# Optimization experiments

Measured on AMD Instinct MI355X. Metric: run time of the kernel, lower is better.

Reference implementation:

```python
import jax, jax.numpy as jnp
import numpy as np

T = 2.0          # hardcoded in the original __init__ (ignores the arg)
EPSILON = 0.1
N_ITERS = 20     # sinkhorn_loss passes n_iters=20 to sinkhorn_normalized
SCALE = 0.001


def setup_inputs() -> dict:
    key = jax.random.key(0)
    k1, k2 = jax.random.split(key)
    B, N, C = 8, 1024, 64
    y_s = jax.random.normal(k1, (B, N, C), dtype=jnp.float32)
    y_t = jax.random.normal(k2, (B, N, C), dtype=jnp.float32)
    return {"y_s": y_s, "y_t": y_t}


def _sinkhorn_loss(x, y):
    # x, y: [N, C]. cdist p=1 -> [N, N]
    Wxy = jnp.sum(jnp.abs(x[:, None, :] - y[None, :, :]), axis=-1)  # [N, N]
    K = jnp.exp(-Wxy / EPSILON)

    def body(P, _):
        P = P / jnp.sum(P, axis=1, keepdims=True)  # row normalize
        P = P / jnp.sum(P, axis=0, keepdims=True)  # col normalize
        return P, None

    P, _ = jax.lax.scan(body, K, None, length=N_ITERS)
    return jnp.sum(P * Wxy)


def reference(y_s, y_t):
    # softmax over dim=1 (the N axis), exactly as nn.Softmax(dim=1) on [B,N,C]
    p_s = jax.nn.softmax(y_s / T, axis=1)
    p_t = jax.nn.softmax(y_t / T, axis=1)
    # original Python loop computes the loss per sample but OVERWRITES
    # emd_loss each iteration; lax.map mirrors the sequential per-sample
    # work, and we return only the last sample's loss (faithful to the bug).
    losses = jax.lax.map(lambda xy: _sinkhorn_loss(xy[0], xy[1]), (p_s, p_t))
    return SCALE * losses[-1]
```

## Files before the change

### kernel.cpp

```cpp
#include <hip/hip_runtime.h>


static constexpr int N = 1024;
static constexpr int C = 64;

static constexpr int WS_XS = 0;
static constexpr int WS_YS = 65536;
static constexpr int WS_K  = 131072;
static constexpr int WS_KT = 1179648;
static constexpr int WS_U  = 2228224;
static constexpr int WS_V  = 2229248;
static constexpr int WS_P  = 2230272;

__device__ __forceinline__ float wsum(float v) {
    #pragma unroll
    for (int o = 32; o > 0; o >>= 1) v += __shfl_down(v, o, 64);
    return v;
}
__device__ __forceinline__ float wmax(float v) {
    #pragma unroll
    for (int o = 32; o > 0; o >>= 1) v = fmaxf(v, __shfl_down(v, o, 64));
    return v;
}

__global__ void __launch_bounds__(256)
softmax_k(const float* __restrict__ ysrc, const float* __restrict__ ytrc,
          float* __restrict__ ws)
{
    __shared__ float sm[4];
    const int tid = threadIdx.x, bid = blockIdx.x;
    const int wid = tid >> 6, lane = tid & 63;
    const float* src = ((bid < C) ? ysrc : ytrc) + 7 * N * C;
    float* dst = ws + ((bid < C) ? WS_XS : WS_YS);
    const int c = bid & (C - 1);

    float vals[4];
    float m = -1e30f;
    #pragma unroll
    for (int q = 0; q < 4; ++q) {
        vals[q] = src[(q * 256 + tid) * C + c] * 0.5f;
        m = fmaxf(m, vals[q]);
    }
    m = wmax(m);
    if (lane == 0) sm[wid] = m;
    __syncthreads();
    m = fmaxf(fmaxf(sm[0], sm[1]), fmaxf(sm[2], sm[3]));
    float s = 0.f;
    #pragma unroll
    for (int q = 0; q < 4; ++q) { vals[q] = expf(vals[q] - m); s += vals[q]; }
    s = wsum(s);
    __syncthreads();
    if (lane == 0) sm[wid] = s;
    __syncthreads();
    s = sm[0] + sm[1] + sm[2] + sm[3];
    const float inv = 1.0f / s;
    #pragma unroll
    for (int q = 0; q < 4; ++q) dst[(q * 256 + tid) * C + c] = vals[q] * inv;
}

__global__ void __launch_bounds__(256)
buildK_k(float* __restrict__ ws)
{
    __shared__ float smem[5184];
    float* xs  = ws + WS_XS;
    float* ysm = ws + WS_YS;
    float* K   = ws + WS_K;
    float* KT  = ws + WS_KT;
    const int tid = threadIdx.x, bid = blockIdx.x;

    if (bid < 4) ws[WS_V + bid * 256 + tid] = 1.0f;

    float* sx = smem;
    float* sy = smem + 2048;
    float* kt = smem + 4128;
    #pragma unroll 1
    for (int t = 0; t < 4; ++t) {
        const int tt = bid * 4 + t;
        const int ti = tt >> 5, tj = tt & 31;
        __syncthreads();
        for (int k = tid; k < 2048; k += 256) sx[k] = xs[ti * 2048 + k];
        for (int k = tid; k < 2048; k += 256)
            sy[(k >> 6) * 65 + (k & 63)] = ysm[tj * 2048 + k];
        __syncthreads();
        float kv[4];
        #pragma unroll
        for (int q = 0; q < 4; ++q) {
            const int idx = q * 256 + tid;
            const int il = idx >> 5, jl = idx & 31;
            float a = 0.f;
            #pragma unroll
            for (int c = 0; c < 64; ++c)
                a += fabsf(sx[il * 64 + c] - sy[jl * 65 + c]);
            kv[q] = expf(-10.0f * a);
            K[(ti * 32 + il) * N + tj * 32 + jl] = kv[q];
        }
        __syncthreads();
        #pragma unroll
        for (int q = 0; q < 4; ++q) {
            const int idx = q * 256 + tid;
            kt[(idx >> 5) * 33 + (idx & 31)] = kv[q];
        }
        __syncthreads();
        #pragma unroll
        for (int q = 0; q < 4; ++q) {
            const int idx = q * 256 + tid;
            const int jl = idx >> 5, il = idx & 31;
            KT[(tj * 32 + jl) * N + ti * 32 + il] = kt[il * 33 + jl];
        }
    }
}

__global__ void __launch_bounds__(256)
rownorm_k(float* __restrict__ ws)
{
    const int r = blockIdx.x * 4 + (threadIdx.x >> 6);
    const int lane = threadIdx.x & 63;
    const float4* Kr4 = (const float4*)(ws + WS_K + r * N);
    const float4* v4  = (const float4*)(ws + WS_V);
    float acc = 0.f;
    #pragma unroll
    for (int j = lane; j < 256; j += 64) {
        const float4 kk = Kr4[j]; const float4 vv = v4[j];
        acc += kk.x * vv.x + kk.y * vv.y + kk.z * vv.z + kk.w * vv.w;
    }
    acc = wsum(acc);
    if (lane == 0) ws[WS_U + r] = 1.0f / acc;
}

__global__ void __launch_bounds__(256)
colnorm_k(float* __restrict__ ws)
{
    const int r = blockIdx.x * 4 + (threadIdx.x >> 6);
    const int lane = threadIdx.x & 63;
    const float4* Kr4 = (const float4*)(ws + WS_KT + r * N);
    const float4* u4  = (const float4*)(ws + WS_U);
    float acc = 0.f;
    #pragma unroll
    for (int j = lane; j < 256; j += 64) {
        const float4 kk = Kr4[j]; const float4 uu = u4[j];
        acc += kk.x * uu.x + kk.y * uu.y + kk.z * uu.z + kk.w * uu.w;
    }
    acc = wsum(acc);
    if (lane == 0) ws[WS_V + r] = 1.0f / acc;
}

__global__ void __launch_bounds__(256)
loss_partial_k(float* __restrict__ ws)
{
    __shared__ float sm[4];
    const int tid = threadIdx.x, bid = blockIdx.x;
    const int wid = tid >> 6, lane = tid & 63;
    const int r = bid * 4 + wid;
    const float* K = ws + WS_K;
    const float* v = ws + WS_V;
    float acc = 0.f;
    for (int j = lane; j < N; j += 64) {
        const float k = K[r * N + j];
        acc += k * v[j] * logf(k);
    }
    acc = wsum(acc);
    if (lane == 0) sm[wid] = ws[WS_U + r] * acc;
    __syncthreads();
    if (tid == 0) ws[WS_P + bid] = sm[0] + sm[1] + sm[2] + sm[3];
}

__global__ void __launch_bounds__(256)
loss_final_k(const float* __restrict__ ws, float* __restrict__ out)
{
    __shared__ float sm[4];
    const int tid = threadIdx.x;
    const int wid = tid >> 6, lane = tid & 63;
    float acc = ws[WS_P + tid];
    acc = wsum(acc);
    if (lane == 0) sm[wid] = acc;
    __syncthreads();
    if (tid == 0)
        out[0] = -1e-4f * (sm[0] + sm[1] + sm[2] + sm[3]);
}

extern "C" void kernel_launch(void* const* d_in, const int* in_sizes, int n_in,
                              void* d_out, int out_size, void* d_ws, size_t ws_size,
                              hipStream_t stream) {
    const float* y_s = (const float*)d_in[0];
    const float* y_t = (const float*)d_in[1];
    float* out = (float*)d_out;
    float* ws  = (float*)d_ws;

    softmax_k<<<dim3(128), dim3(256), 0, stream>>>(y_s, y_t, ws);
    buildK_k<<<dim3(256), dim3(256), 0, stream>>>(ws);
    for (int it = 0; it < 20; ++it) {
        rownorm_k<<<dim3(256), dim3(256), 0, stream>>>(ws);
        colnorm_k<<<dim3(256), dim3(256), 0, stream>>>(ws);
    }
    loss_partial_k<<<dim3(256), dim3(256), 0, stream>>>(ws);
    loss_final_k<<<dim3(1), dim3(256), 0, stream>>>(ws, out);
}
```

Before: 193.5 us.

## Fuse all stages into one persistent kernel with atomic grid barriers

Replaces the 44 separate launches (softmax, K build, 40 row/col normalisations, loss) with a single persistent kernel of 128 blocks that synchronises through an atomic-counter grid barrier, plus a tiny init kernel. Each block now processes twice as many rows and K tiles. This removes launch gaps between dependent tiny kernels. In exchange it halves the parallelism of the K build, relies on all 128 blocks being co-resident, and has a spin guard that could break out early and silently corrupt results.

```diff
diff --git a/kernel.cpp b/kernel.cpp
--- a/kernel.cpp
+++ b/kernel.cpp
@@ -1,16 +1,18 @@
 #include <hip/hip_runtime.h>
 
 
-static constexpr int N = 1024;
-static constexpr int C = 64;
-
-static constexpr int WS_XS = 0;
-static constexpr int WS_YS = 65536;
-static constexpr int WS_K  = 131072;
-static constexpr int WS_KT = 1179648;
-static constexpr int WS_U  = 2228224;
-static constexpr int WS_V  = 2229248;
-static constexpr int WS_P  = 2230272;
+static constexpr int N  = 1024;
+static constexpr int C  = 64;
+static constexpr int NB = 128;
+
+static constexpr int WS_XS  = 0;
+static constexpr int WS_YS  = 65536;
+static constexpr int WS_K   = 131072;
+static constexpr int WS_KT  = 1179648;
+static constexpr int WS_U   = 2228224;
+static constexpr int WS_V   = 2229248;
+static constexpr int WS_P   = 2230272;
+static constexpr int WS_CNT = 2230400;
 
 __device__ __forceinline__ float wsum(float v) {
     #pragma unroll
@@ -24,158 +26,179 @@
 }
 
 __global__ void __launch_bounds__(256)
-softmax_k(const float* __restrict__ ysrc, const float* __restrict__ ytrc,
-          float* __restrict__ ws)
+init_k(float* __restrict__ ws)
 {
-    __shared__ float sm[4];
-    const int tid = threadIdx.x, bid = blockIdx.x;
-    const int wid = tid >> 6, lane = tid & 63;
-    const float* src = ((bid < C) ? ysrc : ytrc) + 7 * N * C;
-    float* dst = ws + ((bid < C) ? WS_XS : WS_YS);
-    const int c = bid & (C - 1);
-
-    float vals[4];
-    float m = -1e30f;
-    #pragma unroll
-    for (int q = 0; q < 4; ++q) {
-        vals[q] = src[(q * 256 + tid) * C + c] * 0.5f;
-        m = fmaxf(m, vals[q]);
-    }
-    m = wmax(m);
-    if (lane == 0) sm[wid] = m;
-    __syncthreads();
-    m = fmaxf(fmaxf(sm[0], sm[1]), fmaxf(sm[2], sm[3]));
-    float s = 0.f;
-    #pragma unroll
-    for (int q = 0; q < 4; ++q) { vals[q] = expf(vals[q] - m); s += vals[q]; }
-    s = wsum(s);
-    __syncthreads();
-    if (lane == 0) sm[wid] = s;
-    __syncthreads();
-    s = sm[0] + sm[1] + sm[2] + sm[3];
-    const float inv = 1.0f / s;
-    #pragma unroll
-    for (int q = 0; q < 4; ++q) dst[(q * 256 + tid) * C + c] = vals[q] * inv;
+    const int tid = threadIdx.x;
+    if (tid == 0) *(int*)(ws + WS_CNT) = 0;
+    for (int i = tid; i < N; i += 256) ws[WS_V + i] = 1.0f;
 }
 
 __global__ void __launch_bounds__(256)
-buildK_k(float* __restrict__ ws)
+sink_k(const float* __restrict__ ysrc, const float* __restrict__ ytrc,
+       float* __restrict__ out, float* __restrict__ ws)
 {
     __shared__ float smem[5184];
-    float* xs  = ws + WS_XS;
-    float* ysm = ws + WS_YS;
-    float* K   = ws + WS_K;
-    float* KT  = ws + WS_KT;
-    const int tid = threadIdx.x, bid = blockIdx.x;
-
-    if (bid < 4) ws[WS_V + bid * 256 + tid] = 1.0f;
-
-    float* sx = smem;
-    float* sy = smem + 2048;
-    float* kt = smem + 4128;
+    const int tid  = threadIdx.x;
+    const int bid  = blockIdx.x;
+    const int wid  = tid >> 6;
+    const int lane = tid & 63;
+    int* cnt = (int*)(ws + WS_CNT);
+    int ep = 0;
+
+    auto gbar = [&]() {
+        __syncthreads();
+        ep += NB;
+        if (tid == 0) {
+            __hip_atomic_fetch_add(cnt, 1, __ATOMIC_RELEASE,
+                                   __HIP_MEMORY_SCOPE_AGENT);
+            int guard = 0;
+            while (__hip_atomic_load(cnt, __ATOMIC_RELAXED,
+                                     __HIP_MEMORY_SCOPE_AGENT) < ep) {
+                __builtin_amdgcn_s_sleep(2);
+                if (++guard > (1 << 22)) break;
+            }
+            __threadfence();
+        }
+        __syncthreads();
+    };
+
+    {
+        const float* src = ((bid < C) ? ysrc : ytrc) + 7 * N * C;
+        float* dst = ws + ((bid < C) ? WS_XS : WS_YS);
+        const int c = bid & (C - 1);
+        float vals[4];
+        float m = -1e30f;
+        #pragma unroll
+        for (int q = 0; q < 4; ++q) {
+            vals[q] = src[(q * 256 + tid) * C + c] * 0.5f;
+            m = fmaxf(m, vals[q]);
+        }
+        m = wmax(m);
+        if (lane == 0) smem[wid] = m;
+        __syncthreads();
+        m = fmaxf(fmaxf(smem[0], smem[1]), fmaxf(smem[2], smem[3]));
+        float s = 0.f;
+        #pragma unroll
+        for (int q = 0; q < 4; ++q) { vals[q] = expf(vals[q] - m); s += vals[q]; }
+        s = wsum(s);
+        __syncthreads();
+        if (lane == 0) smem[wid] = s;
+        __syncthreads();
+        s = smem[0] + smem[1] + smem[2] + smem[3];
+        const float inv = 1.0f / s;
+        #pragma unroll
+        for (int q = 0; q < 4; ++q) dst[(q * 256 + tid) * C + c] = vals[q] * inv;
+    }
+    gbar();
+
+    {
+        float* xs  = ws + WS_XS;
+        float* ysm = ws + WS_YS;
+        float* K   = ws + WS_K;
+        float* KT  = ws + WS_KT;
+        float* sx = smem;
+        float* sy = smem + 2048;
+        float* kt = smem + 4128;
+        #pragma unroll 1
+        for (int t = 0; t < 8; ++t) {
+            const int tt = bid * 8 + t;
+            const int ti = tt >> 5, tj = tt & 31;
+            __syncthreads();
+            for (int k = tid; k < 2048; k += 256) sx[k] = xs[ti * 2048 + k];
+            for (int k = tid; k < 2048; k += 256)
+                sy[(k >> 6) * 65 + (k & 63)] = ysm[tj * 2048 + k];
+            __syncthreads();
+            float kv[4];
+            #pragma unroll
+            for (int q = 0; q < 4; ++q) {
+                const int idx = q * 256 + tid;
+                const int il = idx >> 5, jl = idx & 31;
+                float a = 0.f;
+                #pragma unroll
+                for (int c = 0; c < 64; ++c)
+                    a += fabsf(sx[il * 64 + c] - sy[jl * 65 + c]);
+                kv[q] = expf(-10.0f * a);
+                K[(ti * 32 + il) * N + tj * 32 + jl] = kv[q];
+            }
+            __syncthreads();
+            #pragma unroll
+            for (int q = 0; q < 4; ++q) {
+                const int idx = q * 256 + tid;
+                kt[(idx >> 5) * 33 + (idx & 31)] = kv[q];
+            }
+            __syncthreads();
+            #pragma unroll
+            for (int q = 0; q < 4; ++q) {
+                const int idx = q * 256 + tid;
+                const int jl = idx >> 5, il = idx & 31;
+                KT[(tj * 32 + jl) * N + ti * 32 + il] = kt[il * 33 + jl];
+            }
+        }
+    }
+    gbar();
+
+    const int r0 = bid * 4 + wid;
+    const int r1 = r0 + 512;
+    const float4* K4  = (const float4*)(ws + WS_K);
+    const float4* KT4 = (const float4*)(ws + WS_KT);
+    const float4* v4  = (const float4*)(ws + WS_V);
+    const float4* u4  = (const float4*)(ws + WS_U);
     #pragma unroll 1
-    for (int t = 0; t < 4; ++t) {
-        const int tt = bid * 4 + t;
-        const int ti = tt >> 5, tj = tt & 31;
-        __syncthreads();
-        for (int k = tid; k < 2048; k += 256) sx[k] = xs[ti * 2048 + k];
-        for (int k = tid; k < 2048; k += 256)
-            sy[(k >> 6) * 65 + (k & 63)] = ysm[tj * 2048 + k];
-        __syncthreads();
-        float kv[4];
-        #pragma unroll
-        for (int q = 0; q < 4; ++q) {
-            const int idx = q * 256 + tid;
-            const int il = idx >> 5, jl = idx & 31;
-            float a = 0.f;
-            #pragma unroll
-            for (int c = 0; c < 64; ++c)
-                a += fabsf(sx[il * 64 + c] - sy[jl * 65 + c]);
-            kv[q] = expf(-10.0f * a);
-            K[(ti * 32 + il) * N + tj * 32 + jl] = kv[q];
-        }
-        __syncthreads();
-        #pragma unroll
-        for (int q = 0; q < 4; ++q) {
-            const int idx = q * 256 + tid;
-            kt[(idx >> 5) * 33 + (idx & 31)] = kv[q];
-        }
-        __syncthreads();
-        #pragma unroll
-        for (int q = 0; q < 4; ++q) {
-            const int idx = q * 256 + tid;
-            const int jl = idx >> 5, il = idx & 31;
-            KT[(tj * 32 + jl) * N + ti * 32 + il] = kt[il * 33 + jl];
-        }
-    }
-}
-
-__global__ void __launch_bounds__(256)
-rownorm_k(float* __restrict__ ws)
-{
-    const int r = blockIdx.x * 4 + (threadIdx.x >> 6);
-    const int lane = threadIdx.x & 63;
-    const float4* Kr4 = (const float4*)(ws + WS_K + r * N);
-    const float4* v4  = (const float4*)(ws + WS_V);
-    float acc = 0.f;
-    #pragma unroll
-    for (int j = lane; j < 256; j += 64) {
-        const float4 kk = Kr4[j]; const float4 vv = v4[j];
-        acc += kk.x * vv.x + kk.y * vv.y + kk.z * vv.z + kk.w * vv.w;
-    }
-    acc = wsum(acc);
-    if (lane == 0) ws[WS_U + r] = 1.0f / acc;
-}
-
-__global__ void __launch_bounds__(256)
-colnorm_k(float* __restrict__ ws)
-{
-    const int r = blockIdx.x * 4 + (threadIdx.x >> 6);
-    const int lane = threadIdx.x & 63;
-    const float4* Kr4 = (const float4*)(ws + WS_KT + r * N);
-    const float4* u4  = (const float4*)(ws + WS_U);
-    float acc = 0.f;
-    #pragma unroll
-    for (int j = lane; j < 256; j += 64) {
-        const float4 kk = Kr4[j]; const float4 uu = u4[j];
-        acc += kk.x * uu.x + kk.y * uu.y + kk.z * uu.z + kk.w * uu.w;
-    }
-    acc = wsum(acc);
-    if (lane == 0) ws[WS_V + r] = 1.0f / acc;
-}
-
-__global__ void __launch_bounds__(256)
-loss_partial_k(float* __restrict__ ws)
-{
-    __shared__ float sm[4];
-    const int tid = threadIdx.x, bid = blockIdx.x;
-    const int wid = tid >> 6, lane = tid & 63;
-    const int r = bid * 4 + wid;
-    const float* K = ws + WS_K;
-    const float* v = ws + WS_V;
-    float acc = 0.f;
-    for (int j = lane; j < N; j += 64) {
-        const float k = K[r * N + j];
-        acc += k * v[j] * logf(k);
-    }
-    acc = wsum(acc);
-    if (lane == 0) sm[wid] = ws[WS_U + r] * acc;
-    __syncthreads();
-    if (tid == 0) ws[WS_P + bid] = sm[0] + sm[1] + sm[2] + sm[3];
-}
-
-__global__ void __launch_bounds__(256)
-loss_final_k(const float* __restrict__ ws, float* __restrict__ out)
-{
-    __shared__ float sm[4];
-    const int tid = threadIdx.x;
-    const int wid = tid >> 6, lane = tid & 63;
-    float acc = ws[WS_P + tid];
-    acc = wsum(acc);
-    if (lane == 0) sm[wid] = acc;
-    __syncthreads();
-    if (tid == 0)
-        out[0] = -1e-4f * (sm[0] + sm[1] + sm[2] + sm[3]);
+    for (int it = 0; it < 20; ++it) {
+        float a0 = 0.f, a1 = 0.f;
+        #pragma unroll
+        for (int j = lane; j < 256; j += 64) {
+            const float4 vv = v4[j];
+            const float4 k0 = K4[r0 * 256 + j];
+            const float4 k1 = K4[r1 * 256 + j];
+            a0 += k0.x * vv.x + k0.y * vv.y + k0.z * vv.z + k0.w * vv.w;
+            a1 += k1.x * vv.x + k1.y * vv.y + k1.z * vv.z + k1.w * vv.w;
+        }
+        a0 = wsum(a0); a1 = wsum(a1);
+        if (lane == 0) { ws[WS_U + r0] = 1.0f / a0; ws[WS_U + r1] = 1.0f / a1; }
+        gbar();
+        a0 = 0.f; a1 = 0.f;
+        #pragma unroll
+        for (int j = lane; j < 256; j += 64) {
+            const float4 uu = u4[j];
+            const float4 k0 = KT4[r0 * 256 + j];
+            const float4 k1 = KT4[r1 * 256 + j];
+            a0 += k0.x * uu.x + k0.y * uu.y + k0.z * uu.z + k0.w * uu.w;
+            a1 += k1.x * uu.x + k1.y * uu.y + k1.z * uu.z + k1.w * uu.w;
+        }
+        a0 = wsum(a0); a1 = wsum(a1);
+        if (lane == 0) { ws[WS_V + r0] = 1.0f / a0; ws[WS_V + r1] = 1.0f / a1; }
+        gbar();
+    }
+
+    {
+        const float* K = ws + WS_K;
+        const float* v = ws + WS_V;
+        float a0 = 0.f, a1 = 0.f;
+        for (int j = lane; j < N; j += 64) {
+            const float k0 = K[r0 * N + j];
+            const float k1 = K[r1 * N + j];
+            const float vj = v[j];
+            a0 += k0 * vj * logf(k0);
+            a1 += k1 * vj * logf(k1);
+        }
+        a0 = wsum(a0); a1 = wsum(a1);
+        __syncthreads();
+        if (lane == 0) smem[wid] = ws[WS_U + r0] * a0 + ws[WS_U + r1] * a1;
+        __syncthreads();
+        if (tid == 0) ws[WS_P + bid] = smem[0] + smem[1] + smem[2] + smem[3];
+    }
+    gbar();
+
+    if (bid == 0) {
+        float acc = (tid < NB) ? ws[WS_P + tid] : 0.f;
+        acc = wsum(acc);
+        __syncthreads();
+        if (lane == 0) smem[wid] = acc;
+        __syncthreads();
+        if (tid == 0)
+            out[0] = -1e-4f * (smem[0] + smem[1] + smem[2] + smem[3]);
+    }
 }
 
 extern "C" void kernel_launch(void* const* d_in, const int* in_sizes, int n_in,
@@ -186,12 +209,6 @@
     float* out = (float*)d_out;
     float* ws  = (float*)d_ws;
 
-    softmax_k<<<dim3(128), dim3(256), 0, stream>>>(y_s, y_t, ws);
-    buildK_k<<<dim3(256), dim3(256), 0, stream>>>(ws);
-    for (int it = 0; it < 20; ++it) {
-        rownorm_k<<<dim3(256), dim3(256), 0, stream>>>(ws);
-        colnorm_k<<<dim3(256), dim3(256), 0, stream>>>(ws);
-    }
-    loss_partial_k<<<dim3(256), dim3(256), 0, stream>>>(ws);
-    loss_final_k<<<dim3(1), dim3(256), 0, stream>>>(ws, out);
-}
+    init_k<<<dim3(1),  dim3(256), 0, stream>>>(ws);
+    sink_k<<<dim3(NB), dim3(256), 0, stream>>>(y_s, y_t, out, ws);
+}
```

Measured after the change: 433.7 us. 124% more time.
